# Performance work log

Hardware: AMD Instinct MI355X
Metric: run time of the kernel (lower is better)

Reference implementation:

```python
import jax, jax.numpy as jnp
import numpy as np

B, N, E = 16, 576, 768
H, HID = 12, 768
D = HID // H          # dim_head = 64
SCALE = D ** -0.5
LN_EPS = 1e-5


def setup_inputs() -> dict:
    key = jax.random.key(0)
    ks = jax.random.split(key, 12)
    x = jax.random.normal(ks[0], (B, N, E), jnp.float32)
    dist = jax.random.uniform(ks[1], (N, N), jnp.float32) * 24.0  # pairwise patch distances
    s = E ** -0.5
    return {
        "x": x,
        "dist": dist,
        "ln_g": jnp.ones((E,), jnp.float32),
        "ln_b": jnp.zeros((E,), jnp.float32),
        "Wq": jax.random.normal(ks[2], (E, HID), jnp.float32) * s,
        "bq": jnp.zeros((HID,), jnp.float32),
        "Wk": jax.random.normal(ks[3], (E, HID), jnp.float32) * s,
        "bk": jnp.zeros((HID,), jnp.float32),
        "Wv": jax.random.normal(ks[4], (E, HID), jnp.float32) * s,
        "bv": jnp.zeros((HID,), jnp.float32),
        "Wo": jax.random.normal(ks[5], (HID, E), jnp.float32) * (HID ** -0.5),
        "bo": jnp.zeros((E,), jnp.float32),
        "ak": jax.random.normal(ks[6], (D,), jnp.float32) * 0.1,
        "av": jax.random.normal(ks[7], (D,), jnp.float32) * 0.1,
    }


def _rpe(a, dist):
    # MonotonicallyDecreasingFunctionParallel: per-channel learned decay rate,
    # out[i,j,c] = exp(-softplus(a_c) * dist[i,j])  ->  [N, N, D]
    rate = jax.nn.softplus(a)
    return jnp.exp(-dist[:, :, None] * rate[None, None, :])


def reference(x, dist, ln_g, ln_b, Wq, bq, Wk, bk, Wv, bv, Wo, bo, ak, av):
    b, n = x.shape[0], x.shape[1]
    # LayerNorm
    mu = jnp.mean(x, axis=-1, keepdims=True)
    var = jnp.mean(jnp.square(x - mu), axis=-1, keepdims=True)
    xn = (x - mu) * jax.lax.rsqrt(var + LN_EPS) * ln_g + ln_b
    # projections, then raw row-major reshape [B, H, n, d] (faithful to .view)
    q = (xn @ Wq + bq).reshape(b, H, n, D)
    k = (xn @ Wk + bk).reshape(b, H, n, D)
    v = (xn @ Wv + bv).reshape(b, H, n, D)
    QKT = jnp.einsum("bhnd,bhmd->bhnm", q, k)
    rel_k = _rpe(ak, dist)  # [n, n, D]
    rel_v = _rpe(av, dist)  # [n, n, D]
    # faithful raw reshape [B,H,n,d] -> [n, B*H, d]
    q_r = q.reshape(n, b * H, D)
    QAT = jnp.einsum("nbd,nmd->nbm", q_r, rel_k).reshape(b, H, n, n)
    attn = jax.nn.softmax((QKT + QAT) * SCALE, axis=-1)
    attn_V = jnp.einsum("bhnm,bhmd->bhnd", attn, v)
    attn_r = attn.reshape(n, b * H, n)
    attn_rel_v = jnp.einsum("nbm,nmd->nbd", attn_r, rel_v).reshape(b, H, n, D)
    out = (attn_V + attn_rel_v).reshape(b, n, HID)
    out = out @ Wo + bo  # dropout is identity in eval mode
    return out
```

## Files before the change

kernel.cpp:

```cpp
#include <hip/hip_runtime.h>
#include <hip/hip_fp16.h>

typedef _Float16 f16;
typedef _Float16 v8hf __attribute__((ext_vector_type(8)));
typedef __fp16 v2fp __attribute__((ext_vector_type(2)));
typedef float v4f __attribute__((ext_vector_type(4)));
typedef float v16f __attribute__((ext_vector_type(16)));
typedef unsigned int v4u __attribute__((ext_vector_type(4)));

#define NROW 9216
#define SZH ((size_t)NROW * 768)

__device__ __forceinline__ float softplus_f(float a) {
  return fmaxf(a, 0.f) + log1pf(__expf(-fabsf(a)));
}

__device__ __forceinline__ unsigned int packh(float a, float b) {
  union { v2fp h; unsigned int u; } z;
  z.h = __builtin_amdgcn_cvt_pkrtz(a, b);
  return z.u;
}

__device__ __forceinline__ void gload16(const void* g, void* l) {
  __builtin_amdgcn_global_load_lds(
      (const __attribute__((address_space(1))) unsigned int*)(unsigned long long)g,
      (__attribute__((address_space(3))) unsigned int*)(unsigned int)(unsigned long long)l,
      16, 0, 0);
}

__global__ __launch_bounds__(256) void prep_kernel(
    const float* __restrict__ x, const float* __restrict__ lg, const float* __restrict__ lb,
    const float* __restrict__ Wq, const float* __restrict__ Wk, const float* __restrict__ Wv,
    const float* __restrict__ Wo, const float* __restrict__ ak, const float* __restrict__ av,
    const float* __restrict__ bq, const float* __restrict__ bk, const float* __restrict__ bv,
    f16* __restrict__ xn, f16* __restrict__ wt, float* __restrict__ biasqkv,
    float* __restrict__ rates)
{
  __shared__ float tile[64][65];
  __shared__ float red[8];
  int bid = blockIdx.x, tid = threadIdx.x;
  if (bid < NROW) {
    const float* xr = x + (size_t)bid * 768;
    float v0 = xr[tid], v1 = xr[tid + 256], v2 = xr[tid + 512];
    float s1 = v0 + v1 + v2;
    float s2 = v0 * v0 + v1 * v1 + v2 * v2;
    #pragma unroll
    for (int off = 32; off >= 1; off >>= 1) {
      s1 += __shfl_xor(s1, off);
      s2 += __shfl_xor(s2, off);
    }
    int w = tid >> 6;
    if ((tid & 63) == 0) { red[w] = s1; red[4 + w] = s2; }
    __syncthreads();
    s1 = red[0] + red[1] + red[2] + red[3];
    s2 = red[4] + red[5] + red[6] + red[7];
    float mu = s1 * (1.f / 768.f);
    float var = s2 * (1.f / 768.f) - mu * mu;
    float rs = rsqrtf(var + 1e-5f);
    f16* xo = xn + (size_t)bid * 768;
    xo[tid]       = (f16)((v0 - mu) * rs * lg[tid] + lb[tid]);
    xo[tid + 256] = (f16)((v1 - mu) * rs * lg[tid + 256] + lb[tid + 256]);
    xo[tid + 512] = (f16)((v2 - mu) * rs * lg[tid + 512] + lb[tid + 512]);
    return;
  }
  bid -= NROW;
  if (bid < 576) {
    int wsel = bid / 144, t2 = bid % 144, tr = t2 / 12, tc = t2 % 12;
    const float* W = (wsel == 0) ? Wq : ((wsel == 1) ? Wk : ((wsel == 2) ? Wv : Wo));
    f16* WT = wt + (size_t)wsel * 589824;
    int r = tid >> 2, c0 = (tid & 3) * 16;
    #pragma unroll
    for (int j = 0; j < 16; j++)
      tile[r][c0 + j] = W[(size_t)(tr * 64 + r) * 768 + tc * 64 + c0 + j];
    __syncthreads();
    #pragma unroll
    for (int j = 0; j < 16; j++)
      WT[(size_t)(tc * 64 + r) * 768 + tr * 64 + c0 + j] = (f16)tile[c0 + j][r];
    return;
  }
  if (tid < 64) rates[tid] = softplus_f(ak[tid]);
  else if (tid < 128) rates[tid] = softplus_f(av[tid - 64]);
  for (int i = tid; i < 2304; i += 256)
    biasqkv[i] = (i < 768) ? bq[i] : ((i < 1536) ? bk[i - 768] : bv[i - 1536]);
}

__global__ __launch_bounds__(256) void gemm_kernel(
    const f16* __restrict__ A, const f16* __restrict__ WT,
    const float* __restrict__ bias,
    f16* __restrict__ outh, float* __restrict__ outf, int f32out)
{
  __shared__ __align__(16) f16 At[2][128 * 64];
  __shared__ __align__(16) f16 Bt[2][128 * 64];
  int bid0 = blockIdx.y * gridDim.x + blockIdx.x;
  int nwg = gridDim.x * gridDim.y;
  int nid = (bid0 & 7) * (nwg >> 3) + (bid0 >> 3);
  int cols = gridDim.y;
  int mb = nid / cols, nb = nid % cols;
  int tid = threadIdx.x, lane = tid & 63, w = tid >> 6;
  int wr = w >> 1, wc = w & 1;
  v4f acc[4][4];
  #pragma unroll
  for (int i = 0; i < 4; i++)
    #pragma unroll
    for (int j = 0; j < 4; j++) acc[i][j] = (v4f){0.f, 0.f, 0.f, 0.f};
  int arow0 = mb * 128, brow0 = nb * 128;
  int rb = w * 32 + (lane >> 3);
  int ch = lane & 7;
  auto stage = [&](int buf, int k0) {
    #pragma unroll
    for (int j = 0; j < 4; j++) {
      int row = rb + j * 8;
      int sc = ((ch ^ (row & 7)) << 3);
      gload16(A  + (size_t)(arow0 + row) * 768 + k0 + sc, (char*)At[buf] + w * 4096 + j * 1024);
      gload16(WT + (size_t)(brow0 + row) * 768 + k0 + sc, (char*)Bt[buf] + w * 4096 + j * 1024);
    }
  };
  stage(0, 0);
  for (int ks = 0; ks < 12; ++ks) {
    int cur = ks & 1;
    if (ks < 11) {
      stage(cur ^ 1, (ks + 1) * 64);
      asm volatile("s_waitcnt vmcnt(8)" ::: "memory");
    } else {
      asm volatile("s_waitcnt vmcnt(0)" ::: "memory");
    }
    __builtin_amdgcn_s_barrier();
    __builtin_amdgcn_sched_barrier(0);
    v8hf bf[4][2];
    #pragma unroll
    for (int cf = 0; cf < 4; cf++)
      #pragma unroll
      for (int kk = 0; kk < 2; kk++) {
        int row = wc * 64 + cf * 16 + (lane & 15);
        int bc = kk * 64 + ((lane >> 4) << 4);
        bf[cf][kk] = *(const v8hf*)((char*)Bt[cur] + row * 128 + (bc ^ ((row & 7) << 4)));
      }
    #pragma unroll
    for (int rf = 0; rf < 4; rf++) {
      v8hf af[2];
      int row = wr * 64 + rf * 16 + (lane & 15);
      #pragma unroll
      for (int kk = 0; kk < 2; kk++) {
        int bc = kk * 64 + ((lane >> 4) << 4);
        af[kk] = *(const v8hf*)((char*)At[cur] + row * 128 + (bc ^ ((row & 7) << 4)));
      }
      #pragma unroll
      for (int cf = 0; cf < 4; cf++) {
        acc[rf][cf] = __builtin_amdgcn_mfma_f32_16x16x32_f16(af[0], bf[cf][0], acc[rf][cf], 0, 0, 0);
        acc[rf][cf] = __builtin_amdgcn_mfma_f32_16x16x32_f16(af[1], bf[cf][1], acc[rf][cf], 0, 0, 0);
      }
    }
    __builtin_amdgcn_sched_barrier(0);
    __builtin_amdgcn_s_barrier();
  }
  #pragma unroll
  for (int cf = 0; cf < 4; cf++) {
    int col = nb * 128 + wc * 64 + cf * 16 + (lane & 15);
    float bb = bias[col];
    int z = col / 768;
    int colz = col - z * 768;
    #pragma unroll
    for (int rf = 0; rf < 4; rf++) {
      int row0 = mb * 128 + wr * 64 + rf * 16 + ((lane >> 4) << 2);
      #pragma unroll
      for (int r = 0; r < 4; r++) {
        float val = acc[rf][cf][r] + bb;
        if (f32out) outf[(size_t)(row0 + r) * 768 + col] = val;
        else outh[(size_t)z * SZH + (size_t)(row0 + r) * 768 + colz] = (f16)val;
      }
    }
  }
}

__global__ __launch_bounds__(256) void vt_kernel(const f16* __restrict__ vw, f16* __restrict__ vt)
{
  __shared__ f16 tile[64][72];
  int g = blockIdx.x, tc = blockIdx.y;
  int tid = threadIdx.x;
  int tr = tid >> 2, c16 = (tid & 3) * 16;
  const f16* src = vw + (size_t)g * 36864 + (size_t)(tc * 64 + tr) * 64 + c16;
  *(v8hf*)&tile[tr][c16] = *(const v8hf*)src;
  *(v8hf*)&tile[tr][c16 + 8] = *(const v8hf*)(src + 8);
  __syncthreads();
  int d = tid >> 2, t16 = (tid & 3) * 16;
  f16 outv[16];
  #pragma unroll
  for (int j = 0; j < 16; j++) outv[j] = tile[t16 + j][d];
  f16* dst = vt + (size_t)g * 36864 + (size_t)d * 576 + tc * 64 + t16;
  *(v8hf*)dst = *(v8hf*)outv;
  *(v8hf*)(dst + 8) = *(v8hf*)(outv + 8);
}

__global__ __launch_bounds__(384, 3) void attn_kernel(
    const f16* __restrict__ qw, const f16* __restrict__ kw, const f16* __restrict__ vt,
    const float* __restrict__ dist, const float* __restrict__ rates,
    f16* __restrict__ aw, f16* __restrict__ parth, float* __restrict__ ml, int nslice)
{
  __shared__ __align__(16) f16 Ke[64 * 64];
  __shared__ __align__(16) f16 Vt[64 * 64];
  __shared__ float dl[576];
  __shared__ float rkv[128];
  int gc = (blockIdx.x & 7) * 72 + (blockIdx.x >> 3);
  int sl = blockIdx.y;
  int g = gc / 3, c = gc - g * 3;
  int tid = threadIdx.x, lane = tid & 63, w = tid >> 6;
  int l31 = lane & 31, h = lane >> 5;
  int ntile = 9 / nslice;
  size_t hbase = (size_t)g * 36864;
  if (tid < 128) rkv[tid] = rates[tid];
  for (int t = tid; t < ntile * 64; t += 384)
    dl[t] = dist[(size_t)gc * 576 + sl * ntile * 64 + t];
  __syncthreads();
  v8hf qf[4];
  {
    const f16* qp = qw + hbase + (size_t)(c * 192 + w * 32 + l31) * 64 + h * 8;
    #pragma unroll
    for (int kk = 0; kk < 4; kk++) {
      v8hf v = *(const v8hf*)(qp + kk * 16);
      #pragma unroll
      for (int j = 0; j < 8; j++) v[j] = v[j] * (f16)0.125f;
      qf[kk] = v;
    }
  }
  v16f o0, o1;
  #pragma unroll
  for (int i = 0; i < 16; i++) { o0[i] = 0.f; o1[i] = 0.f; }
  float mrun = -1e30f, lrun = 0.f;
  for (int t = 0; t < ntile; ++t) {
    int mbase = sl * ntile * 64 + t * 64;
    int mloc = t * 64;
    for (int u = tid; u < 1024; u += 384) {
      if (u < 512) {
        int mm = u >> 3, d8 = (u & 7) * 8;
        float dv = dl[mloc + mm];
        v8hf kv = *(const v8hf*)(kw + hbase + (size_t)(mbase + mm) * 64 + d8);
        #pragma unroll
        for (int j = 0; j < 8; j++)
          kv[j] = (f16)((float)kv[j] + __expf(-rkv[d8 + j] * dv));
        *(v8hf*)((char*)Ke + mm * 128 + ((d8 * 2) ^ ((mm & 7) << 4))) = kv;
      } else {
        int uu = u - 512;
        int dd = uu >> 3, m8 = (uu & 7) * 8;
        float rv = rkv[64 + dd];
        v8hf vv = *(const v8hf*)(vt + hbase + (size_t)dd * 576 + mbase + m8);
        #pragma unroll
        for (int j = 0; j < 8; j++)
          vv[j] = (f16)((float)vv[j] + __expf(-rv * dl[mloc + m8 + j]));
        *(v8hf*)((char*)Vt + dd * 128 + ((m8 * 2) ^ ((dd & 7) << 4))) = vv;
      }
    }
    __syncthreads();
    v16f s0, s1;
    #pragma unroll
    for (int i = 0; i < 16; i++) { s0[i] = 0.f; s1[i] = 0.f; }
    #pragma unroll
    for (int kk = 0; kk < 4; kk++) {
      int bc = kk * 32 + h * 16;
      int sw0 = (l31 & 7) << 4;
      v8hf a0 = *(const v8hf*)((char*)Ke + l31 * 128 + (bc ^ sw0));
      v8hf a1 = *(const v8hf*)((char*)Ke + (32 + l31) * 128 + (bc ^ sw0));
      s0 = __builtin_amdgcn_mfma_f32_32x32x16_f16(a0, qf[kk], s0, 0, 0, 0);
      s1 = __builtin_amdgcn_mfma_f32_32x32x16_f16(a1, qf[kk], s1, 0, 0, 0);
    }
    float tmax = s0[0];
    #pragma unroll
    for (int i = 1; i < 16; i++) tmax = fmaxf(tmax, s0[i]);
    #pragma unroll
    for (int i = 0; i < 16; i++) tmax = fmaxf(tmax, s1[i]);
    tmax = fmaxf(tmax, __shfl_xor(tmax, 32));
    if (!__all(tmax - mrun <= 8.f)) {
      float mnew = fmaxf(mrun, tmax);
      float alpha = __expf(mrun - mnew);
      lrun *= alpha;
      #pragma unroll
      for (int i = 0; i < 16; i++) { o0[i] *= alpha; o1[i] *= alpha; }
      mrun = mnew;
    }
    float rs = 0.f;
    #pragma unroll
    for (int i = 0; i < 16; i++) { float p = __expf(s0[i] - mrun); s0[i] = p; rs += p; }
    #pragma unroll
    for (int i = 0; i < 16; i++) { float p = __expf(s1[i] - mrun); s1[i] = p; rs += p; }
    rs += __shfl_xor(rs, 32);
    lrun += rs;
    unsigned int Wd[16], Xd[16];
    #pragma unroll
    for (int i = 0; i < 8; i++) {
      Wd[i]     = packh(s0[2 * i], s0[2 * i + 1]);
      Wd[8 + i] = packh(s1[2 * i], s1[2 * i + 1]);
    }
    #pragma unroll
    for (int i = 0; i < 16; i++) Xd[i] = __shfl_xor((int)Wd[i], 32);
    v4u fw[4];
    fw[0] = h ? (v4u){Xd[2],  Xd[3],  Wd[2],  Wd[3]}  : (v4u){Wd[0],  Wd[1],  Xd[0],  Xd[1]};
    fw[1] = h ? (v4u){Xd[6],  Xd[7],  Wd[6],  Wd[7]}  : (v4u){Wd[4],  Wd[5],  Xd[4],  Xd[5]};
    fw[2] = h ? (v4u){Xd[10], Xd[11], Wd[10], Wd[11]} : (v4u){Wd[8],  Wd[9],  Xd[8],  Xd[9]};
    fw[3] = h ? (v4u){Xd[14], Xd[15], Wd[14], Wd[15]} : (v4u){Wd[12], Wd[13], Xd[12], Xd[13]};
    #pragma unroll
    for (int kk = 0; kk < 4; kk++) {
      int bc = kk * 32 + h * 16;
      int sw0 = (l31 & 7) << 4;
      v8hf a0 = *(const v8hf*)((char*)Vt + l31 * 128 + (bc ^ sw0));
      v8hf a1 = *(const v8hf*)((char*)Vt + (32 + l31) * 128 + (bc ^ sw0));
      union { v4u u; v8hf hh; } pb;
      pb.u = fw[kk];
      o0 = __builtin_amdgcn_mfma_f32_32x32x16_f16(a0, pb.hh, o0, 0, 0, 0);
      o1 = __builtin_amdgcn_mfma_f32_32x32x16_f16(a1, pb.hh, o1, 0, 0, 0);
    }
    __syncthreads();
  }
  float inv = 1.f / lrun;
  if (nslice == 1) {
    f16* ap = aw + hbase + (size_t)(c * 192 + w * 32 + l31) * 64;
    #pragma unroll
    for (int r = 0; r < 16; r++) {
      int d = (r & 3) + 8 * (r >> 2) + 4 * h;
      ap[d]      = (f16)(o0[r] * inv);
      ap[d + 32] = (f16)(o1[r] * inv);
    }
  } else {
    f16* pp = parth + ((size_t)sl * 576 + gc) * 12288;
    int q = w * 32 + l31;
    #pragma unroll
    for (int r = 0; r < 16; r++) {
      int d = (r & 3) + 8 * (r >> 2) + 4 * h;
      pp[d * 192 + q]        = (f16)(o0[r] * inv);
      pp[(d + 32) * 192 + q] = (f16)(o1[r] * inv);
    }
    if (h == 0) {
      float* mlp = ml + ((size_t)sl * 576 + gc) * 384;
      mlp[q]       = mrun;
      mlp[192 + q] = lrun;
    }
  }
}

__global__ __launch_bounds__(192) void comb_kernel(
    const f16* __restrict__ parth, const float* __restrict__ ml, f16* __restrict__ aw)
{
  int gc = blockIdx.x;
  int q = threadIdx.x;
  int g = gc / 3, c = gc - g * 3;
  float mv[3], lv[3];
  float M = -1e30f;
  #pragma unroll
  for (int s = 0; s < 3; s++) {
    const float* mlp = ml + ((size_t)s * 576 + gc) * 384;
    mv[s] = mlp[q];
    lv[s] = mlp[192 + q];
    M = fmaxf(M, mv[s]);
  }
  float L = 0.f, wgt[3];
  #pragma unroll
  for (int s = 0; s < 3; s++) { wgt[s] = lv[s] * __expf(mv[s] - M); L += wgt[s]; }
  float invL = 1.f / L;
  #pragma unroll
  for (int s = 0; s < 3; s++) wgt[s] *= invL;
  f16 row[64];
  #pragma unroll
  for (int d = 0; d < 64; d++) {
    float a = 0.f;
    #pragma unroll
    for (int s = 0; s < 3; s++)
      a += wgt[s] * (float)parth[((size_t)s * 576 + gc) * 12288 + d * 192 + q];
    row[d] = (f16)a;
  }
  f16* ap = aw + (size_t)g * 36864 + (size_t)(c * 192 + q) * 64;
  #pragma unroll
  for (int j = 0; j < 8; j++) *(v8hf*)(ap + j * 8) = *(v8hf*)(row + j * 8);
}

extern "C" void kernel_launch(void* const* d_in, const int* in_sizes, int n_in,
                              void* d_out, int out_size, void* d_ws, size_t ws_size,
                              hipStream_t stream) {
  const float* x    = (const float*)d_in[0];
  const float* dist = (const float*)d_in[1];
  const float* lg   = (const float*)d_in[2];
  const float* lb   = (const float*)d_in[3];
  const float* Wq   = (const float*)d_in[4];
  const float* bq   = (const float*)d_in[5];
  const float* Wk   = (const float*)d_in[6];
  const float* bk   = (const float*)d_in[7];
  const float* Wv   = (const float*)d_in[8];
  const float* bv   = (const float*)d_in[9];
  const float* Wo   = (const float*)d_in[10];
  const float* bo   = (const float*)d_in[11];
  const float* ak   = (const float*)d_in[12];
  const float* av   = (const float*)d_in[13];

  f16* ws = (f16*)d_ws;
  f16* xn = ws;
  f16* qw = ws + SZH;
  f16* kw = ws + 2 * SZH;
  f16* vw = ws + 3 * SZH;
  f16* wt = ws + 4 * SZH;
  float* fbase   = (float*)(wt + 4 * 589824);
  float* biasqkv = fbase;
  float* rates   = fbase + 2304;
  f16* parth     = (f16*)(fbase + 2432);
  float* mlb     = (float*)(parth + (size_t)3 * 576 * 12288);
  f16* vtb = xn;
  f16* aw  = vw;

  size_t need_split = ((size_t)4 * SZH + 4 * 589824 + (size_t)3 * 576 * 12288) * 2
                    + ((size_t)2432 + (size_t)3 * 576 * 384) * 4;
  int ns = (ws_size >= need_split) ? 3 : 1;

  prep_kernel<<<9216 + 576 + 1, 256, 0, stream>>>(x, lg, lb, Wq, Wk, Wv, Wo, ak, av,
                                                  bq, bk, bv, xn, wt, biasqkv, rates);
  gemm_kernel<<<dim3(72, 18), 256, 0, stream>>>(xn, wt, biasqkv, qw, nullptr, 0);
  vt_kernel<<<dim3(192, 9), 256, 0, stream>>>(vw, vtb);
  attn_kernel<<<dim3(576, ns), 384, 0, stream>>>(qw, kw, vtb, dist, rates, aw, parth, mlb, ns);
  if (ns > 1)
    comb_kernel<<<576, 192, 0, stream>>>(parth, mlb, aw);
  gemm_kernel<<<dim3(72, 6), 256, 0, stream>>>(aw, wt + 3 * 589824, bo, nullptr, (float*)d_out, 1);
}
```

Measured before the change: 167.2 us.

## Prefetch next K/V tile into registers, vectorize LayerNorm, restructure GEMM barriers

The attention kernel now issues the global loads for the next K/V tile into registers right after the LDS barrier, so they overlap the current tile's MFMA and softmax work instead of stalling at the top of each iteration. It also raises wave priority around the MFMA blocks and drops the final redundant barrier. The LayerNorm prep now uses float4 loads and half4 stores on 192 threads. The GEMM loop moves its wait and barrier to the end of each iteration with a full vmcnt(0) wait, which may cut overlap of the double-buffered loads.

Result: slower. 177.3 us (+6.0%).

```diff
diff --git a/kernel.cpp b/kernel.cpp
--- a/kernel.cpp
+++ b/kernel.cpp
@@ -2,6 +2,7 @@
 #include <hip/hip_fp16.h>
 
 typedef _Float16 f16;
+typedef _Float16 v4hf __attribute__((ext_vector_type(4)));
 typedef _Float16 v8hf __attribute__((ext_vector_type(8)));
 typedef __fp16 v2fp __attribute__((ext_vector_type(2)));
 typedef float v4f __attribute__((ext_vector_type(4)));
@@ -41,9 +42,10 @@
   int bid = blockIdx.x, tid = threadIdx.x;
   if (bid < NROW) {
     const float* xr = x + (size_t)bid * 768;
-    float v0 = xr[tid], v1 = xr[tid + 256], v2 = xr[tid + 512];
-    float s1 = v0 + v1 + v2;
-    float s2 = v0 * v0 + v1 * v1 + v2 * v2;
+    float4 v = make_float4(0.f, 0.f, 0.f, 0.f);
+    if (tid < 192) v = *(const float4*)(xr + tid * 4);
+    float s1 = v.x + v.y + v.z + v.w;
+    float s2 = v.x * v.x + v.y * v.y + v.z * v.z + v.w * v.w;
     #pragma unroll
     for (int off = 32; off >= 1; off >>= 1) {
       s1 += __shfl_xor(s1, off);
@@ -57,10 +59,16 @@
     float mu = s1 * (1.f / 768.f);
     float var = s2 * (1.f / 768.f) - mu * mu;
     float rs = rsqrtf(var + 1e-5f);
-    f16* xo = xn + (size_t)bid * 768;
-    xo[tid]       = (f16)((v0 - mu) * rs * lg[tid] + lb[tid]);
-    xo[tid + 256] = (f16)((v1 - mu) * rs * lg[tid + 256] + lb[tid + 256]);
-    xo[tid + 512] = (f16)((v2 - mu) * rs * lg[tid + 512] + lb[tid + 512]);
+    if (tid < 192) {
+      float4 gg = *(const float4*)(lg + tid * 4);
+      float4 bb = *(const float4*)(lb + tid * 4);
+      v4hf o;
+      o[0] = (f16)((v.x - mu) * rs * gg.x + bb.x);
+      o[1] = (f16)((v.y - mu) * rs * gg.y + bb.y);
+      o[2] = (f16)((v.z - mu) * rs * gg.z + bb.z);
+      o[3] = (f16)((v.w - mu) * rs * gg.w + bb.w);
+      *(v4hf*)(xn + (size_t)bid * 768 + tid * 4) = o;
+    }
     return;
   }
   bid -= NROW;
@@ -116,16 +124,12 @@
     }
   };
   stage(0, 0);
+  asm volatile("s_waitcnt vmcnt(0)" ::: "memory");
+  __builtin_amdgcn_s_barrier();
+  __builtin_amdgcn_sched_barrier(0);
   for (int ks = 0; ks < 12; ++ks) {
     int cur = ks & 1;
-    if (ks < 11) {
-      stage(cur ^ 1, (ks + 1) * 64);
-      asm volatile("s_waitcnt vmcnt(8)" ::: "memory");
-    } else {
-      asm volatile("s_waitcnt vmcnt(0)" ::: "memory");
-    }
-    __builtin_amdgcn_s_barrier();
-    __builtin_amdgcn_sched_barrier(0);
+    if (ks < 11) stage(cur ^ 1, (ks + 1) * 64);
     v8hf bf[4][2];
     #pragma unroll
     for (int cf = 0; cf < 4; cf++)
@@ -151,7 +155,11 @@
       }
     }
     __builtin_amdgcn_sched_barrier(0);
-    __builtin_amdgcn_s_barrier();
+    if (ks < 11) {
+      asm volatile("s_waitcnt vmcnt(0)" ::: "memory");
+      __builtin_amdgcn_s_barrier();
+      __builtin_amdgcn_sched_barrier(0);
+    }
   }
   #pragma unroll
   for (int cf = 0; cf < 4; cf++) {
@@ -210,7 +218,37 @@
   if (tid < 128) rkv[tid] = rates[tid];
   for (int t = tid; t < ntile * 64; t += 384)
     dl[t] = dist[(size_t)gc * 576 + sl * ntile * 64 + t];
-  __syncthreads();
+
+  auto gptr = [&](int u, int mbase) -> const v8hf* {
+    if (u < 512) {
+      int mm = u >> 3, d8 = (u & 7) * 8;
+      return (const v8hf*)(kw + hbase + (size_t)(mbase + mm) * 64 + d8);
+    }
+    int uu = u - 512;
+    int dd = uu >> 3, m8 = (uu & 7) * 8;
+    return (const v8hf*)(vt + hbase + (size_t)dd * 576 + mbase + m8);
+  };
+  auto wchunk = [&](int u, int mloc, v8hf raw) {
+    if (u < 512) {
+      int mm = u >> 3, d8 = (u & 7) * 8;
+      float dv = dl[mloc + mm];
+      v8hf kv;
+      #pragma unroll
+      for (int j = 0; j < 8; j++)
+        kv[j] = (f16)((float)raw[j] + __expf(-rkv[d8 + j] * dv));
+      *(v8hf*)((char*)Ke + mm * 128 + ((d8 * 2) ^ ((mm & 7) << 4))) = kv;
+    } else {
+      int uu = u - 512;
+      int dd = uu >> 3, m8 = (uu & 7) * 8;
+      float rv = rkv[64 + dd];
+      v8hf vv;
+      #pragma unroll
+      for (int j = 0; j < 8; j++)
+        vv[j] = (f16)((float)raw[j] + __expf(-rv * dl[mloc + m8 + j]));
+      *(v8hf*)((char*)Vt + dd * 128 + ((m8 * 2) ^ ((dd & 7) << 4))) = vv;
+    }
+  };
+
   v8hf qf[4];
   {
     const f16* qp = qw + hbase + (size_t)(c * 192 + w * 32 + l31) * 64 + h * 8;
@@ -222,37 +260,34 @@
       qf[kk] = v;
     }
   }
+  v8hf r0, r1, r2 = {};
+  {
+    int mb0 = sl * ntile * 64;
+    r0 = *gptr(tid, mb0);
+    r1 = *gptr(tid + 384, mb0);
+    if (tid < 256) r2 = *gptr(tid + 768, mb0);
+  }
   v16f o0, o1;
   #pragma unroll
   for (int i = 0; i < 16; i++) { o0[i] = 0.f; o1[i] = 0.f; }
   float mrun = -1e30f, lrun = 0.f;
+  __syncthreads();
   for (int t = 0; t < ntile; ++t) {
-    int mbase = sl * ntile * 64 + t * 64;
     int mloc = t * 64;
-    for (int u = tid; u < 1024; u += 384) {
-      if (u < 512) {
-        int mm = u >> 3, d8 = (u & 7) * 8;
-        float dv = dl[mloc + mm];
-        v8hf kv = *(const v8hf*)(kw + hbase + (size_t)(mbase + mm) * 64 + d8);
-        #pragma unroll
-        for (int j = 0; j < 8; j++)
-          kv[j] = (f16)((float)kv[j] + __expf(-rkv[d8 + j] * dv));
-        *(v8hf*)((char*)Ke + mm * 128 + ((d8 * 2) ^ ((mm & 7) << 4))) = kv;
-      } else {
-        int uu = u - 512;
-        int dd = uu >> 3, m8 = (uu & 7) * 8;
-        float rv = rkv[64 + dd];
-        v8hf vv = *(const v8hf*)(vt + hbase + (size_t)dd * 576 + mbase + m8);
-        #pragma unroll
-        for (int j = 0; j < 8; j++)
-          vv[j] = (f16)((float)vv[j] + __expf(-rv * dl[mloc + m8 + j]));
-        *(v8hf*)((char*)Vt + dd * 128 + ((m8 * 2) ^ ((dd & 7) << 4))) = vv;
-      }
-    }
+    wchunk(tid, mloc, r0);
+    wchunk(tid + 384, mloc, r1);
+    if (tid < 256) wchunk(tid + 768, mloc, r2);
     __syncthreads();
+    if (t + 1 < ntile) {
+      int mb2 = sl * ntile * 64 + (t + 1) * 64;
+      r0 = *gptr(tid, mb2);
+      r1 = *gptr(tid + 384, mb2);
+      if (tid < 256) r2 = *gptr(tid + 768, mb2);
+    }
     v16f s0, s1;
     #pragma unroll
     for (int i = 0; i < 16; i++) { s0[i] = 0.f; s1[i] = 0.f; }
+    __builtin_amdgcn_s_setprio(1);
     #pragma unroll
     for (int kk = 0; kk < 4; kk++) {
       int bc = kk * 32 + h * 16;
@@ -262,6 +297,7 @@
       s0 = __builtin_amdgcn_mfma_f32_32x32x16_f16(a0, qf[kk], s0, 0, 0, 0);
       s1 = __builtin_amdgcn_mfma_f32_32x32x16_f16(a1, qf[kk], s1, 0, 0, 0);
     }
+    __builtin_amdgcn_s_setprio(0);
     float tmax = s0[0];
     #pragma unroll
     for (int i = 1; i < 16; i++) tmax = fmaxf(tmax, s0[i]);
@@ -296,6 +332,7 @@
     fw[1] = h ? (v4u){Xd[6],  Xd[7],  Wd[6],  Wd[7]}  : (v4u){Wd[4],  Wd[5],  Xd[4],  Xd[5]};
     fw[2] = h ? (v4u){Xd[10], Xd[11], Wd[10], Wd[11]} : (v4u){Wd[8],  Wd[9],  Xd[8],  Xd[9]};
     fw[3] = h ? (v4u){Xd[14], Xd[15], Wd[14], Wd[15]} : (v4u){Wd[12], Wd[13], Xd[12], Xd[13]};
+    __builtin_amdgcn_s_setprio(1);
     #pragma unroll
     for (int kk = 0; kk < 4; kk++) {
       int bc = kk * 32 + h * 16;
@@ -307,7 +344,8 @@
       o0 = __builtin_amdgcn_mfma_f32_32x32x16_f16(a0, pb.hh, o0, 0, 0, 0);
       o1 = __builtin_amdgcn_mfma_f32_32x32x16_f16(a1, pb.hh, o1, 0, 0, 0);
     }
-    __syncthreads();
+    __builtin_amdgcn_s_setprio(0);
+    if (t + 1 < ntile) __syncthreads();
   }
   float inv = 1.f / lrun;
   if (nslice == 1) {
```

## Halve GEMM K-tile, add narrow-N variant for output projection, vectorize LayerNorm

Applied to the files above, without the earlier changes.

The GEMM is templated on column fragments per wave and its K-step drops from 64 to 32, which halves LDS use and lets launch bounds ask for 4 waves per SIMD. The LDS swizzle is changed to match the 64-byte rows. The output projection uses a 64-wide N tile, doubling its grid from 432 to 864 blocks to fill more CUs. LayerNorm in the prep kernel now uses float4 loads and half4 stores over 192 threads. The cost is twice as many barriers and K iterations, with less data reuse per stage.

Result: slower. 175.3 us (+4.8%).

```diff
diff --git a/kernel.cpp b/kernel.cpp
--- a/kernel.cpp
+++ b/kernel.cpp
@@ -2,6 +2,7 @@
 #include <hip/hip_fp16.h>
 
 typedef _Float16 f16;
+typedef _Float16 v4hf __attribute__((ext_vector_type(4)));
 typedef _Float16 v8hf __attribute__((ext_vector_type(8)));
 typedef __fp16 v2fp __attribute__((ext_vector_type(2)));
 typedef float v4f __attribute__((ext_vector_type(4)));
@@ -41,9 +42,10 @@
   int bid = blockIdx.x, tid = threadIdx.x;
   if (bid < NROW) {
     const float* xr = x + (size_t)bid * 768;
-    float v0 = xr[tid], v1 = xr[tid + 256], v2 = xr[tid + 512];
-    float s1 = v0 + v1 + v2;
-    float s2 = v0 * v0 + v1 * v1 + v2 * v2;
+    float4 v = make_float4(0.f, 0.f, 0.f, 0.f);
+    if (tid < 192) v = *(const float4*)(xr + tid * 4);
+    float s1 = v.x + v.y + v.z + v.w;
+    float s2 = v.x * v.x + v.y * v.y + v.z * v.z + v.w * v.w;
     #pragma unroll
     for (int off = 32; off >= 1; off >>= 1) {
       s1 += __shfl_xor(s1, off);
@@ -57,10 +59,16 @@
     float mu = s1 * (1.f / 768.f);
     float var = s2 * (1.f / 768.f) - mu * mu;
     float rs = rsqrtf(var + 1e-5f);
-    f16* xo = xn + (size_t)bid * 768;
-    xo[tid]       = (f16)((v0 - mu) * rs * lg[tid] + lb[tid]);
-    xo[tid + 256] = (f16)((v1 - mu) * rs * lg[tid + 256] + lb[tid + 256]);
-    xo[tid + 512] = (f16)((v2 - mu) * rs * lg[tid + 512] + lb[tid + 512]);
+    if (tid < 192) {
+      float4 gg = *(const float4*)(lg + tid * 4);
+      float4 bb = *(const float4*)(lb + tid * 4);
+      v4hf o;
+      o[0] = (f16)((v.x - mu) * rs * gg.x + bb.x);
+      o[1] = (f16)((v.y - mu) * rs * gg.y + bb.y);
+      o[2] = (f16)((v.z - mu) * rs * gg.z + bb.z);
+      o[3] = (f16)((v.w - mu) * rs * gg.w + bb.w);
+      *(v4hf*)(xn + (size_t)bid * 768 + tid * 4) = o;
+    }
     return;
   }
   bid -= NROW;
@@ -84,13 +92,16 @@
     biasqkv[i] = (i < 768) ? bq[i] : ((i < 1536) ? bk[i - 768] : bv[i - 1536]);
 }
 
-__global__ __launch_bounds__(256) void gemm_kernel(
+template<int CF>
+__global__ __launch_bounds__(256, 4) void gemm_kernel(
     const f16* __restrict__ A, const f16* __restrict__ WT,
     const float* __restrict__ bias,
     f16* __restrict__ outh, float* __restrict__ outf, int f32out)
 {
-  __shared__ __align__(16) f16 At[2][128 * 64];
-  __shared__ __align__(16) f16 Bt[2][128 * 64];
+  constexpr int BN = CF * 32;
+  constexpr int SL = 2 + CF / 2;
+  __shared__ __align__(16) f16 At[2][128 * 32];
+  __shared__ __align__(16) f16 Bt[2][BN * 32];
   int bid0 = blockIdx.y * gridDim.x + blockIdx.x;
   int nwg = gridDim.x * gridDim.y;
   int nid = (bid0 & 7) * (nwg >> 3) + (bid0 >> 3);
@@ -98,64 +109,72 @@
   int mb = nid / cols, nb = nid % cols;
   int tid = threadIdx.x, lane = tid & 63, w = tid >> 6;
   int wr = w >> 1, wc = w & 1;
-  v4f acc[4][4];
+  v4f acc[4][CF];
   #pragma unroll
   for (int i = 0; i < 4; i++)
     #pragma unroll
-    for (int j = 0; j < 4; j++) acc[i][j] = (v4f){0.f, 0.f, 0.f, 0.f};
-  int arow0 = mb * 128, brow0 = nb * 128;
-  int rb = w * 32 + (lane >> 3);
-  int ch = lane & 7;
+    for (int j = 0; j < CF; j++) acc[i][j] = (v4f){0.f, 0.f, 0.f, 0.f};
+  int arow0 = mb * 128, brow0 = nb * BN;
+  int rsub = lane >> 2;
+  int sl = lane & 3;
   auto stage = [&](int buf, int k0) {
     #pragma unroll
-    for (int j = 0; j < 4; j++) {
-      int row = rb + j * 8;
-      int sc = ((ch ^ (row & 7)) << 3);
-      gload16(A  + (size_t)(arow0 + row) * 768 + k0 + sc, (char*)At[buf] + w * 4096 + j * 1024);
-      gload16(WT + (size_t)(brow0 + row) * 768 + k0 + sc, (char*)Bt[buf] + w * 4096 + j * 1024);
+    for (int j = 0; j < 2; j++) {
+      int row = w * 32 + j * 16 + rsub;
+      int g = sl ^ ((row ^ (row >> 2)) & 3);
+      gload16(A + (size_t)(arow0 + row) * 768 + k0 + g * 8,
+              (char*)At[buf] + w * 2048 + j * 1024);
+    }
+    if constexpr (CF == 4) {
+      #pragma unroll
+      for (int j = 0; j < 2; j++) {
+        int row = w * 32 + j * 16 + rsub;
+        int g = sl ^ ((row ^ (row >> 2)) & 3);
+        gload16(WT + (size_t)(brow0 + row) * 768 + k0 + g * 8,
+                (char*)Bt[buf] + w * 2048 + j * 1024);
+      }
+    } else {
+      int row = w * 16 + rsub;
+      int g = sl ^ ((row ^ (row >> 2)) & 3);
+      gload16(WT + (size_t)(brow0 + row) * 768 + k0 + g * 8,
+              (char*)Bt[buf] + w * 1024);
     }
   };
   stage(0, 0);
-  for (int ks = 0; ks < 12; ++ks) {
+  for (int ks = 0; ks < 24; ++ks) {
     int cur = ks & 1;
-    if (ks < 11) {
-      stage(cur ^ 1, (ks + 1) * 64);
-      asm volatile("s_waitcnt vmcnt(8)" ::: "memory");
+    if (ks < 23) {
+      stage(cur ^ 1, (ks + 1) * 32);
+      if constexpr (CF == 4) asm volatile("s_waitcnt vmcnt(4)" ::: "memory");
+      else                   asm volatile("s_waitcnt vmcnt(3)" ::: "memory");
     } else {
       asm volatile("s_waitcnt vmcnt(0)" ::: "memory");
     }
     __builtin_amdgcn_s_barrier();
     __builtin_amdgcn_sched_barrier(0);
-    v8hf bf[4][2];
-    #pragma unroll
-    for (int cf = 0; cf < 4; cf++)
+    int gch = lane >> 4;
+    v8hf bf[CF];
+    #pragma unroll
+    for (int cf = 0; cf < CF; cf++) {
+      int row = wc * (CF * 16) + cf * 16 + (lane & 15);
+      int slot = gch ^ ((row ^ (row >> 2)) & 3);
+      bf[cf] = *(const v8hf*)((char*)Bt[cur] + row * 64 + slot * 16);
+    }
+    #pragma unroll
+    for (int rf = 0; rf < 4; rf++) {
+      int row = wr * 64 + rf * 16 + (lane & 15);
+      int slot = gch ^ ((row ^ (row >> 2)) & 3);
+      v8hf af = *(const v8hf*)((char*)At[cur] + row * 64 + slot * 16);
       #pragma unroll
-      for (int kk = 0; kk < 2; kk++) {
-        int row = wc * 64 + cf * 16 + (lane & 15);
-        int bc = kk * 64 + ((lane >> 4) << 4);
-        bf[cf][kk] = *(const v8hf*)((char*)Bt[cur] + row * 128 + (bc ^ ((row & 7) << 4)));
-      }
-    #pragma unroll
-    for (int rf = 0; rf < 4; rf++) {
-      v8hf af[2];
-      int row = wr * 64 + rf * 16 + (lane & 15);
-      #pragma unroll
-      for (int kk = 0; kk < 2; kk++) {
-        int bc = kk * 64 + ((lane >> 4) << 4);
-        af[kk] = *(const v8hf*)((char*)At[cur] + row * 128 + (bc ^ ((row & 7) << 4)));
-      }
-      #pragma unroll
-      for (int cf = 0; cf < 4; cf++) {
-        acc[rf][cf] = __builtin_amdgcn_mfma_f32_16x16x32_f16(af[0], bf[cf][0], acc[rf][cf], 0, 0, 0);
-        acc[rf][cf] = __builtin_amdgcn_mfma_f32_16x16x32_f16(af[1], bf[cf][1], acc[rf][cf], 0, 0, 0);
-      }
+      for (int cf = 0; cf < CF; cf++)
+        acc[rf][cf] = __builtin_amdgcn_mfma_f32_16x16x32_f16(af, bf[cf], acc[rf][cf], 0, 0, 0);
     }
     __builtin_amdgcn_sched_barrier(0);
     __builtin_amdgcn_s_barrier();
   }
   #pragma unroll
-  for (int cf = 0; cf < 4; cf++) {
-    int col = nb * 128 + wc * 64 + cf * 16 + (lane & 15);
+  for (int cf = 0; cf < CF; cf++) {
+    int col = nb * BN + wc * (CF * 16) + cf * 16 + (lane & 15);
     float bb = bias[col];
     int z = col / 768;
     int colz = col - z * 768;
@@ -408,10 +427,10 @@
 
   prep_kernel<<<9216 + 576 + 1, 256, 0, stream>>>(x, lg, lb, Wq, Wk, Wv, Wo, ak, av,
                                                   bq, bk, bv, xn, wt, biasqkv, rates);
-  gemm_kernel<<<dim3(72, 18), 256, 0, stream>>>(xn, wt, biasqkv, qw, nullptr, 0);
+  gemm_kernel<4><<<dim3(72, 18), 256, 0, stream>>>(xn, wt, biasqkv, qw, nullptr, 0);
   vt_kernel<<<dim3(192, 9), 256, 0, stream>>>(vw, vtb);
   attn_kernel<<<dim3(576, ns), 384, 0, stream>>>(qw, kw, vtb, dist, rates, aw, parth, mlb, ns);
   if (ns > 1)
     comb_kernel<<<576, 192, 0, stream>>>(parth, mlb, aw);
-  gemm_kernel<<<dim3(72, 6), 256, 0, stream>>>(aw, wt + 3 * 589824, bo, nullptr, (float*)d_out, 1);
-}
+  gemm_kernel<2><<<dim3(72, 12), 256, 0, stream>>>(aw, wt + 3 * 589824, bo, nullptr, (float*)d_out, 1);
+}
```

## Replace split-KV attention with smaller query-chunk blocks and drop combine kernel

Applied to the files above, without the earlier changes.

The attention kernel no longer splits the key range into three slices plus a separate combine pass. Instead each block handles 96 query rows with 192 threads over all 9 key tiles, giving 1152 blocks at a higher occupancy bound. This removes the partial-output writes, the m/l buffers and the extra combine launch. In exchange each block regenerates the K and V tiles with the positional-decay terms for only half as many queries, doubling that exp-heavy staging work overall. The LayerNorm prep also switches to float4 loads and packed half stores, and the final barrier in the tile loop is skipped.

Result: slower. 227.1 us (+35.8%).

```diff
diff --git a/kernel.cpp b/kernel.cpp
--- a/kernel.cpp
+++ b/kernel.cpp
@@ -2,6 +2,7 @@
 #include <hip/hip_fp16.h>
 
 typedef _Float16 f16;
+typedef _Float16 v4hf __attribute__((ext_vector_type(4)));
 typedef _Float16 v8hf __attribute__((ext_vector_type(8)));
 typedef __fp16 v2fp __attribute__((ext_vector_type(2)));
 typedef float v4f __attribute__((ext_vector_type(4)));
@@ -41,9 +42,10 @@
   int bid = blockIdx.x, tid = threadIdx.x;
   if (bid < NROW) {
     const float* xr = x + (size_t)bid * 768;
-    float v0 = xr[tid], v1 = xr[tid + 256], v2 = xr[tid + 512];
-    float s1 = v0 + v1 + v2;
-    float s2 = v0 * v0 + v1 * v1 + v2 * v2;
+    float4 v = make_float4(0.f, 0.f, 0.f, 0.f);
+    if (tid < 192) v = *(const float4*)(xr + tid * 4);
+    float s1 = v.x + v.y + v.z + v.w;
+    float s2 = v.x * v.x + v.y * v.y + v.z * v.z + v.w * v.w;
     #pragma unroll
     for (int off = 32; off >= 1; off >>= 1) {
       s1 += __shfl_xor(s1, off);
@@ -57,10 +59,16 @@
     float mu = s1 * (1.f / 768.f);
     float var = s2 * (1.f / 768.f) - mu * mu;
     float rs = rsqrtf(var + 1e-5f);
-    f16* xo = xn + (size_t)bid * 768;
-    xo[tid]       = (f16)((v0 - mu) * rs * lg[tid] + lb[tid]);
-    xo[tid + 256] = (f16)((v1 - mu) * rs * lg[tid + 256] + lb[tid + 256]);
-    xo[tid + 512] = (f16)((v2 - mu) * rs * lg[tid + 512] + lb[tid + 512]);
+    if (tid < 192) {
+      float4 gg = *(const float4*)(lg + tid * 4);
+      float4 bb = *(const float4*)(lb + tid * 4);
+      v4hf o;
+      o[0] = (f16)((v.x - mu) * rs * gg.x + bb.x);
+      o[1] = (f16)((v.y - mu) * rs * gg.y + bb.y);
+      o[2] = (f16)((v.z - mu) * rs * gg.z + bb.z);
+      o[3] = (f16)((v.w - mu) * rs * gg.w + bb.w);
+      *(v4hf*)(xn + (size_t)bid * 768 + tid * 4) = o;
+    }
     return;
   }
   bid -= NROW;
@@ -191,29 +199,29 @@
   *(v8hf*)(dst + 8) = *(v8hf*)(outv + 8);
 }
 
-__global__ __launch_bounds__(384, 3) void attn_kernel(
+__global__ __launch_bounds__(192, 6) void attn_kernel(
     const f16* __restrict__ qw, const f16* __restrict__ kw, const f16* __restrict__ vt,
     const float* __restrict__ dist, const float* __restrict__ rates,
-    f16* __restrict__ aw, f16* __restrict__ parth, float* __restrict__ ml, int nslice)
+    f16* __restrict__ aw)
 {
   __shared__ __align__(16) f16 Ke[64 * 64];
   __shared__ __align__(16) f16 Vt[64 * 64];
   __shared__ float dl[576];
   __shared__ float rkv[128];
-  int gc = (blockIdx.x & 7) * 72 + (blockIdx.x >> 3);
-  int sl = blockIdx.y;
-  int g = gc / 3, c = gc - g * 3;
+  int bid = blockIdx.x;
+  int nid = (bid & 7) * 144 + (bid >> 3);
+  int g = nid / 6, qc = nid - g * 6;
+  int gc = 3 * g + (qc >> 1);
   int tid = threadIdx.x, lane = tid & 63, w = tid >> 6;
   int l31 = lane & 31, h = lane >> 5;
-  int ntile = 9 / nslice;
   size_t hbase = (size_t)g * 36864;
   if (tid < 128) rkv[tid] = rates[tid];
-  for (int t = tid; t < ntile * 64; t += 384)
-    dl[t] = dist[(size_t)gc * 576 + sl * ntile * 64 + t];
+  for (int t = tid; t < 576; t += 192)
+    dl[t] = dist[(size_t)gc * 576 + t];
   __syncthreads();
   v8hf qf[4];
   {
-    const f16* qp = qw + hbase + (size_t)(c * 192 + w * 32 + l31) * 64 + h * 8;
+    const f16* qp = qw + hbase + (size_t)(qc * 96 + w * 32 + l31) * 64 + h * 8;
     #pragma unroll
     for (int kk = 0; kk < 4; kk++) {
       v8hf v = *(const v8hf*)(qp + kk * 16);
@@ -226,13 +234,12 @@
   #pragma unroll
   for (int i = 0; i < 16; i++) { o0[i] = 0.f; o1[i] = 0.f; }
   float mrun = -1e30f, lrun = 0.f;
-  for (int t = 0; t < ntile; ++t) {
-    int mbase = sl * ntile * 64 + t * 64;
-    int mloc = t * 64;
-    for (int u = tid; u < 1024; u += 384) {
+  for (int t = 0; t < 9; ++t) {
+    int mbase = t * 64;
+    for (int u = tid; u < 1024; u += 192) {
       if (u < 512) {
         int mm = u >> 3, d8 = (u & 7) * 8;
-        float dv = dl[mloc + mm];
+        float dv = dl[mbase + mm];
         v8hf kv = *(const v8hf*)(kw + hbase + (size_t)(mbase + mm) * 64 + d8);
         #pragma unroll
         for (int j = 0; j < 8; j++)
@@ -245,7 +252,7 @@
         v8hf vv = *(const v8hf*)(vt + hbase + (size_t)dd * 576 + mbase + m8);
         #pragma unroll
         for (int j = 0; j < 8; j++)
-          vv[j] = (f16)((float)vv[j] + __expf(-rv * dl[mloc + m8 + j]));
+          vv[j] = (f16)((float)vv[j] + __expf(-rv * dl[mbase + m8 + j]));
         *(v8hf*)((char*)Vt + dd * 128 + ((m8 * 2) ^ ((dd & 7) << 4))) = vv;
       }
     }
@@ -307,67 +314,16 @@
       o0 = __builtin_amdgcn_mfma_f32_32x32x16_f16(a0, pb.hh, o0, 0, 0, 0);
       o1 = __builtin_amdgcn_mfma_f32_32x32x16_f16(a1, pb.hh, o1, 0, 0, 0);
     }
-    __syncthreads();
+    if (t < 8) __syncthreads();
   }
   float inv = 1.f / lrun;
-  if (nslice == 1) {
-    f16* ap = aw + hbase + (size_t)(c * 192 + w * 32 + l31) * 64;
-    #pragma unroll
-    for (int r = 0; r < 16; r++) {
-      int d = (r & 3) + 8 * (r >> 2) + 4 * h;
-      ap[d]      = (f16)(o0[r] * inv);
-      ap[d + 32] = (f16)(o1[r] * inv);
-    }
-  } else {
-    f16* pp = parth + ((size_t)sl * 576 + gc) * 12288;
-    int q = w * 32 + l31;
-    #pragma unroll
-    for (int r = 0; r < 16; r++) {
-      int d = (r & 3) + 8 * (r >> 2) + 4 * h;
-      pp[d * 192 + q]        = (f16)(o0[r] * inv);
-      pp[(d + 32) * 192 + q] = (f16)(o1[r] * inv);
-    }
-    if (h == 0) {
-      float* mlp = ml + ((size_t)sl * 576 + gc) * 384;
-      mlp[q]       = mrun;
-      mlp[192 + q] = lrun;
-    }
-  }
-}
-
-__global__ __launch_bounds__(192) void comb_kernel(
-    const f16* __restrict__ parth, const float* __restrict__ ml, f16* __restrict__ aw)
-{
-  int gc = blockIdx.x;
-  int q = threadIdx.x;
-  int g = gc / 3, c = gc - g * 3;
-  float mv[3], lv[3];
-  float M = -1e30f;
-  #pragma unroll
-  for (int s = 0; s < 3; s++) {
-    const float* mlp = ml + ((size_t)s * 576 + gc) * 384;
-    mv[s] = mlp[q];
-    lv[s] = mlp[192 + q];
-    M = fmaxf(M, mv[s]);
-  }
-  float L = 0.f, wgt[3];
-  #pragma unroll
-  for (int s = 0; s < 3; s++) { wgt[s] = lv[s] * __expf(mv[s] - M); L += wgt[s]; }
-  float invL = 1.f / L;
-  #pragma unroll
-  for (int s = 0; s < 3; s++) wgt[s] *= invL;
-  f16 row[64];
-  #pragma unroll
-  for (int d = 0; d < 64; d++) {
-    float a = 0.f;
-    #pragma unroll
-    for (int s = 0; s < 3; s++)
-      a += wgt[s] * (float)parth[((size_t)s * 576 + gc) * 12288 + d * 192 + q];
-    row[d] = (f16)a;
-  }
-  f16* ap = aw + (size_t)g * 36864 + (size_t)(c * 192 + q) * 64;
-  #pragma unroll
-  for (int j = 0; j < 8; j++) *(v8hf*)(ap + j * 8) = *(v8hf*)(row + j * 8);
+  f16* ap = aw + hbase + (size_t)(qc * 96 + w * 32 + l31) * 64;
+  #pragma unroll
+  for (int r = 0; r < 16; r++) {
+    int d = (r & 3) + 8 * (r >> 2) + 4 * h;
+    ap[d]      = (f16)(o0[r] * inv);
+    ap[d + 32] = (f16)(o1[r] * inv);
+  }
 }
 
 extern "C" void kernel_launch(void* const* d_in, const int* in_sizes, int n_in,
@@ -397,21 +353,13 @@
   float* fbase   = (float*)(wt + 4 * 589824);
   float* biasqkv = fbase;
   float* rates   = fbase + 2304;
-  f16* parth     = (f16*)(fbase + 2432);
-  float* mlb     = (float*)(parth + (size_t)3 * 576 * 12288);
   f16* vtb = xn;
   f16* aw  = vw;
-
-  size_t need_split = ((size_t)4 * SZH + 4 * 589824 + (size_t)3 * 576 * 12288) * 2
-                    + ((size_t)2432 + (size_t)3 * 576 * 384) * 4;
-  int ns = (ws_size >= need_split) ? 3 : 1;
 
   prep_kernel<<<9216 + 576 + 1, 256, 0, stream>>>(x, lg, lb, Wq, Wk, Wv, Wo, ak, av,
                                                   bq, bk, bv, xn, wt, biasqkv, rates);
   gemm_kernel<<<dim3(72, 18), 256, 0, stream>>>(xn, wt, biasqkv, qw, nullptr, 0);
   vt_kernel<<<dim3(192, 9), 256, 0, stream>>>(vw, vtb);
-  attn_kernel<<<dim3(576, ns), 384, 0, stream>>>(qw, kw, vtb, dist, rates, aw, parth, mlb, ns);
-  if (ns > 1)
-    comb_kernel<<<576, 192, 0, stream>>>(parth, mlb, aw);
+  attn_kernel<<<1152, 192, 0, stream>>>(qw, kw, vtb, dist, rates, aw);
   gemm_kernel<<<dim3(72, 6), 256, 0, stream>>>(aw, wt + 3 * 589824, bo, nullptr, (float*)d_out, 1);
 }
```
